# Performance work log

Hardware: AMD Instinct MI355X
Metric: run time of the kernel (lower is better)

Reference implementation:

```python
import jax, jax.numpy as jnp
import numpy as np

WS = 8
NH = 8
C = 192
HD = C // NH
SCALE = HD ** -0.5
EPS = 1e-5


def setup_inputs() -> dict:
    key = jax.random.key(0)
    ks = jax.random.split(key, 7)
    B, H, W = 8, 256, 256
    x = jax.random.normal(ks[0], (B, C, H, W), dtype=jnp.float32)
    gamma = jnp.ones((C,), dtype=jnp.float32)
    beta = jnp.zeros((C,), dtype=jnp.float32)
    w_qkv = jax.random.normal(ks[1], (C, 3 * C), dtype=jnp.float32) * (C ** -0.5)
    b_qkv = jnp.zeros((3 * C,), dtype=jnp.float32)
    w_proj = jax.random.normal(ks[2], (C, C), dtype=jnp.float32) * (C ** -0.5)
    b_proj = jnp.zeros((C,), dtype=jnp.float32)
    return {"x": x, "gamma": gamma, "beta": beta, "w_qkv": w_qkv,
            "b_qkv": b_qkv, "w_proj": w_proj, "b_proj": b_proj}


def reference(x, gamma, beta, w_qkv, b_qkv, w_proj, b_proj):
    B, Cc, H, W = x.shape
    # H, W chosen divisible by WS -> pad branch is a no-op
    nh, nw = H // WS, W // WS
    # window partition: [B,C,H,W] -> [B*nh*nw, WS*WS, C]
    xw = x.reshape(B, Cc, nh, WS, nw, WS)
    xw = xw.transpose(0, 2, 4, 3, 5, 1).reshape(-1, WS * WS, Cc)
    # LayerNorm over channel dim
    mu = xw.mean(axis=-1, keepdims=True)
    var = jnp.mean((xw - mu) ** 2, axis=-1, keepdims=True)
    xn = (xw - mu) * jax.lax.rsqrt(var + EPS) * gamma + beta
    # QKV projection -> [3, nWin, NH, S, HD]
    S = WS * WS
    qkv = (xn @ w_qkv + b_qkv).reshape(-1, S, 3, NH, HD)
    qkv = qkv.transpose(2, 0, 3, 1, 4)
    q, k, v = qkv[0], qkv[1], qkv[2]
    attn = jax.nn.softmax(jnp.einsum('whsd,whtd->whst', q, k) * SCALE, axis=-1)
    xa = jnp.einsum('whst,whtd->whsd', attn, v)
    xa = xa.transpose(0, 2, 1, 3).reshape(-1, S, Cc)
    xa = xa @ w_proj + b_proj
    # un-window: -> [B, C, H, W]
    xa = xa.reshape(B, nh, nw, WS, WS, Cc)
    xa = xa.transpose(0, 5, 1, 3, 2, 4).reshape(B, Cc, H, W)
    return jax.nn.sigmoid(xa.mean(axis=1, keepdims=True))
```

## Files before the change

kernel.cpp:

```cpp
#include <hip/hip_runtime.h>
#include <hip/hip_bf16.h>


typedef __attribute__((ext_vector_type(4))) float floatx4;
typedef __attribute__((ext_vector_type(8))) short short8;

#define SCALE_Q 0.20412414523193154f
#define LN_EPS 1e-5f

#define RXN 200
#define RQK 264
#define RPC 40
#define OFF_XN    0
#define OFF_Q     25600
#define OFF_K     59392
#define OFF_PC    93184
#define OFF_LOGIT 134144
#define OFF_VW    134400
#define LDS_BYTES 136448

__device__ __forceinline__ floatx4 mfma16(short8 a, short8 b, floatx4 c) {
  return __builtin_amdgcn_mfma_f32_16x16x32_bf16(a, b, c, 0, 0, 0);
}

__global__ void prep_kernel(const float* __restrict__ w_qkv,
                            const float* __restrict__ w_proj,
                            const float* __restrict__ b_proj,
                            __hip_bfloat16* __restrict__ wfrag,
                            float* __restrict__ wbar) {
  int tid = blockIdx.x * 256 + threadIdx.x;
  if (tid < 36 * 6 * 64) {
    int j = tid / 384, rem = tid % 384, ksr = rem / 64, l = rem % 64;
    int n  = 16 * j + (l & 15);
    int k0 = 32 * ksr + (l >> 4) * 8;
#pragma unroll
    for (int i = 0; i < 8; ++i)
      wfrag[(size_t)tid * 8 + i] = __float2bfloat16(w_qkv[(k0 + i) * 576 + n]);
  }
  if (tid < 192) {
    float s = 0.f;
    for (int c = 0; c < 192; ++c) s += w_proj[tid * 192 + c];
    wbar[tid] = s * (1.f / 192.f);
  } else if (tid == 192) {
    float s = 0.f;
    for (int c = 0; c < 192; ++c) s += b_proj[c];
    wbar[192] = s * (1.f / 192.f);
  }
}

__global__ __launch_bounds__(512, 2) void swin_kernel(
    const float* __restrict__ x,
    const float* __restrict__ gamma,
    const float* __restrict__ beta,
    const float* __restrict__ b_qkv,
    const __hip_bfloat16* __restrict__ wfrag,
    const float* __restrict__ wbar,
    float* __restrict__ out) {
  __shared__ __align__(16) char smem[LDS_BYTES];
  __hip_bfloat16* xn = (__hip_bfloat16*)(smem + OFF_XN);
  __hip_bfloat16* lq = (__hip_bfloat16*)(smem + OFF_Q);
  __hip_bfloat16* lk = (__hip_bfloat16*)(smem + OFF_K);
  float* logit = (float*)(smem + OFF_LOGIT);
  float* vwf   = (float*)(smem + OFF_VW);
  float2* scratch = (float2*)(smem + OFF_PC);

  const int tid = threadIdx.x;
  const int w   = tid >> 6;
  const int l   = tid & 63;
  const int l15 = l & 15;
  const int lg  = l >> 4;
  __hip_bfloat16* pcw = (__hip_bfloat16*)(smem + OFF_PC + w * (64 * RPC * 2));
  const floatx4 fzero = {0.f, 0.f, 0.f, 0.f};

  for (int i = tid; i < 64 * 64; i += 512) {
    int rr = i >> 6, hc = i & 63;
    int hh = hc >> 3, dd = 24 + (hc & 7);
    lq[rr * RQK + hh * 32 + dd] = __float2bfloat16(0.f);
    lk[rr * RQK + hh * 32 + dd] = __float2bfloat16(0.f);
  }
  if (tid < 64) logit[tid] = 0.f;
  vwf[tid] = 0.f;
  __syncthreads();

  const int p  = blockIdx.x;
  const int bb = p & 7;
  const int wh = p >> 3;
  const int tr = l >> 3, tc = l & 7;
  const int c0 = w * 24;
  const float* xb = x + (size_t)bb * 192 * 65536 + (size_t)(wh * 8 + tr) * 256 + tc;

  float xr[24];
#pragma unroll
  for (int i = 0; i < 24; ++i) xr[i] = xb[(size_t)(c0 + i) * 65536];

#pragma unroll 1
  for (int it = 0; it < 32; ++it) {
    float s1 = 0.f, s2 = 0.f;
#pragma unroll
    for (int i = 0; i < 24; ++i) { s1 += xr[i]; s2 += xr[i] * xr[i]; }
    scratch[w * 64 + l] = make_float2(s1, s2);
    __syncthreads();
    float ts = 0.f, tq = 0.f;
#pragma unroll
    for (int g = 0; g < 8; ++g) { float2 v = scratch[g * 64 + l]; ts += v.x; tq += v.y; }
    const float mu   = ts * (1.f / 192.f);
    const float rstd = rsqrtf(tq * (1.f / 192.f) - mu * mu + LN_EPS);
#pragma unroll
    for (int i = 0; i < 24; ++i) {
      float xv = (xr[i] - mu) * rstd * gamma[c0 + i] + beta[c0 + i];
      xn[l * RXN + c0 + i] = __float2bfloat16(xv);
    }
    __syncthreads();

    if (it < 31) {
#pragma unroll
      for (int i = 0; i < 24; ++i)
        xr[i] = xb[(size_t)(c0 + i) * 65536 + (it + 1) * 8];
    }

    short8 af[4][6];
#pragma unroll
    for (int mi = 0; mi < 4; ++mi)
#pragma unroll
      for (int ks = 0; ks < 6; ++ks)
        af[mi][ks] = *(const short8*)&xn[(16 * mi + l15) * RXN + 32 * ks + lg * 8];

    for (int j = w; j < 36; j += 8) {
      floatx4 aa[4];
#pragma unroll
      for (int mi = 0; mi < 4; ++mi) aa[mi] = fzero;
      const short8* bp = (const short8*)wfrag + (size_t)(j * 384 + l);
#pragma unroll
      for (int ks = 0; ks < 6; ++ks) {
        short8 bf = bp[ks * 64];
#pragma unroll
        for (int mi = 0; mi < 4; ++mi) aa[mi] = mfma16(af[mi][ks], bf, aa[mi]);
      }
      const int n = 16 * j + l15;
      const float bias = b_qkv[n];
      if (j < 12) {
        const int hh = n / 24, dd = n - hh * 24;
#pragma unroll
        for (int mi = 0; mi < 4; ++mi)
#pragma unroll
          for (int rg = 0; rg < 4; ++rg) {
            int t = 16 * mi + lg * 4 + rg;
            lq[t * RQK + hh * 32 + dd] = __float2bfloat16((aa[mi][rg] + bias) * SCALE_Q);
          }
      } else if (j < 24) {
        const int cc = n - 192;
        const int hh = cc / 24, dd = cc - hh * 24;
#pragma unroll
        for (int mi = 0; mi < 4; ++mi)
#pragma unroll
          for (int rg = 0; rg < 4; ++rg) {
            int t = 16 * mi + lg * 4 + rg;
            lk[t * RQK + hh * 32 + dd] = __float2bfloat16(aa[mi][rg] + bias);
          }
      } else {
        const int cc = n - 384;
        const int hh = cc / 24;
        const float wbv = wbar[cc];
        float part[16];
#pragma unroll
        for (int mi = 0; mi < 4; ++mi)
#pragma unroll
          for (int rg = 0; rg < 4; ++rg)
            part[mi * 4 + rg] = (aa[mi][rg] + bias) * wbv;
#pragma unroll
        for (int v2 = 0; v2 < 16; ++v2) {
          float t0 = part[v2];
          t0 += __shfl_xor(t0, 1);
          t0 += __shfl_xor(t0, 2);
          t0 += __shfl_xor(t0, 4);
          part[v2] = t0;
        }
        if ((l15 & 7) == 0) {
#pragma unroll
          for (int mi = 0; mi < 4; ++mi)
#pragma unroll
            for (int rg = 0; rg < 4; ++rg) {
              int t = 16 * mi + lg * 4 + rg;
              atomicAdd(&vwf[hh * 64 + t], part[mi * 4 + rg]);
            }
        }
      }
    }
    __syncthreads();

    {
      const int hh = w;
      short8 qf[4], kf[4];
#pragma unroll
      for (int i = 0; i < 4; ++i) {
        qf[i] = *(const short8*)&lq[(16 * i + l15) * RQK + hh * 32 + lg * 8];
        kf[i] = *(const short8*)&lk[(16 * i + l15) * RQK + hh * 32 + lg * 8];
      }
      floatx4 sc[4][4];
#pragma unroll
      for (int i = 0; i < 4; ++i)
#pragma unroll
        for (int j2 = 0; j2 < 4; ++j2)
          sc[i][j2] = mfma16(qf[i], kf[j2], fzero);
#pragma unroll
      for (int i = 0; i < 4; ++i)
#pragma unroll
        for (int j2 = 0; j2 < 4; ++j2)
#pragma unroll
          for (int rg = 0; rg < 4; ++rg)
            sc[i][j2][rg] = exp2f(sc[i][j2][rg] * 1.44269504f);

      short8 vwfrag[2], onesf;
#pragma unroll
      for (int q2 = 0; q2 < 8; ++q2) onesf[q2] = (short)0x3F80;
#pragma unroll
      for (int kc = 0; kc < 2; ++kc)
#pragma unroll
        for (int q2 = 0; q2 < 8; ++q2) {
          __hip_bfloat16 hb = __float2bfloat16(vwf[hh * 64 + kc * 32 + lg * 8 + q2]);
          short sv; __builtin_memcpy(&sv, &hb, 2);
          vwfrag[kc][q2] = sv;
        }

      floatx4 cacc[4], racc[4];
#pragma unroll
      for (int i = 0; i < 4; ++i) { cacc[i] = fzero; racc[i] = fzero; }
#pragma unroll
      for (int kc = 0; kc < 2; ++kc) {
#pragma unroll
        for (int i = 0; i < 4; ++i)
#pragma unroll
          for (int jj = 0; jj < 2; ++jj)
#pragma unroll
            for (int rg = 0; rg < 4; ++rg) {
              int row = 16 * i + lg * 4 + rg;
              pcw[row * RPC + jj * 16 + l15] = __float2bfloat16(sc[i][kc * 2 + jj][rg]);
            }
#pragma unroll
        for (int i = 0; i < 4; ++i) {
          short8 pf = *(const short8*)&pcw[(16 * i + l15) * RPC + lg * 8];
          cacc[i] = mfma16(pf, vwfrag[kc], cacc[i]);
          racc[i] = mfma16(pf, onesf, racc[i]);
        }
      }
      if (l15 == 0) {
#pragma unroll
        for (int i = 0; i < 4; ++i)
#pragma unroll
          for (int rg = 0; rg < 4; ++rg) {
            int row = 16 * i + lg * 4 + rg;
            atomicAdd(&logit[row], cacc[i][rg] / racc[i][rg]);
          }
      }
    }
    __syncthreads();

    if (tid < 64) {
      float vL = logit[tid] + wbar[192];
      out[(size_t)bb * 65536 + (size_t)(wh * 8 + (tid >> 3)) * 256 + it * 8 + (tid & 7)]
          = 1.f / (1.f + __expf(-vL));
      logit[tid] = 0.f;
    }
    vwf[tid] = 0.f;
  }
}

extern "C" void kernel_launch(void* const* d_in, const int* in_sizes, int n_in,
                              void* d_out, int out_size, void* d_ws, size_t ws_size,
                              hipStream_t stream) {
  const float* x      = (const float*)d_in[0];
  const float* gamma  = (const float*)d_in[1];
  const float* beta   = (const float*)d_in[2];
  const float* w_qkv  = (const float*)d_in[3];
  const float* b_qkv  = (const float*)d_in[4];
  const float* w_proj = (const float*)d_in[5];
  const float* b_proj = (const float*)d_in[6];
  float* out = (float*)d_out;

  __hip_bfloat16* wfrag = (__hip_bfloat16*)d_ws;
  float* wbar = (float*)((char*)d_ws + 221184);

  prep_kernel<<<54, 256, 0, stream>>>(w_qkv, w_proj, b_proj, wfrag, wbar);
  swin_kernel<<<256, 512, 0, stream>>>(x, gamma, beta, b_qkv, wfrag, wbar, out);
}
```

Before: 1.184 ms.

## Shrink LDS footprint, split row strips across more blocks, replace PV MFMA with shuffles

Aliases the normalized-input buffer onto the Q region and the LayerNorm scratch onto K, and drops the per-wave P staging buffer and logit buffer. This roughly halves LDS so more blocks fit per CU, and the launch-bounds hint is raised to match. The grid doubles by splitting each window row into two halves, giving 512 blocks instead of 256 on a large-CU GPU. The attention-times-vw reduction now uses FMAs and cross-lane shuffles instead of bf16 MFMA through LDS, the next-input prefetch moves after the QKV GEMM, and zero padding is rewritten every iteration. The risks are extra barriers per iteration and register pressure under the tighter occupancy bound.

```diff
diff --git a/kernel.cpp b/kernel.cpp
--- a/kernel.cpp
+++ b/kernel.cpp
@@ -10,14 +10,10 @@
 
 #define RXN 200
 #define RQK 264
-#define RPC 40
-#define OFF_XN    0
-#define OFF_Q     25600
-#define OFF_K     59392
-#define OFF_PC    93184
-#define OFF_LOGIT 134144
-#define OFF_VW    134400
-#define LDS_BYTES 136448
+#define OFF_Q  0
+#define OFF_K  33792
+#define OFF_VW 67584
+#define LDS_BYTES 69632
 
 __device__ __forceinline__ floatx4 mfma16(short8 a, short8 b, floatx4 c) {
   return __builtin_amdgcn_mfma_f32_16x16x32_bf16(a, b, c, 0, 0, 0);
@@ -48,7 +44,7 @@
   }
 }
 
-__global__ __launch_bounds__(512, 2) void swin_kernel(
+__global__ __launch_bounds__(512, 4) void swin_kernel(
     const float* __restrict__ x,
     const float* __restrict__ gamma,
     const float* __restrict__ beta,
@@ -57,44 +53,34 @@
     const float* __restrict__ wbar,
     float* __restrict__ out) {
   __shared__ __align__(16) char smem[LDS_BYTES];
-  __hip_bfloat16* xn = (__hip_bfloat16*)(smem + OFF_XN);
+  __hip_bfloat16* xn = (__hip_bfloat16*)(smem + OFF_Q);
   __hip_bfloat16* lq = (__hip_bfloat16*)(smem + OFF_Q);
   __hip_bfloat16* lk = (__hip_bfloat16*)(smem + OFF_K);
-  float* logit = (float*)(smem + OFF_LOGIT);
-  float* vwf   = (float*)(smem + OFF_VW);
-  float2* scratch = (float2*)(smem + OFF_PC);
+  float* vwf = (float*)(smem + OFF_VW);
+  float2* scratch = (float2*)(smem + OFF_K);
 
   const int tid = threadIdx.x;
   const int w   = tid >> 6;
   const int l   = tid & 63;
   const int l15 = l & 15;
   const int lg  = l >> 4;
-  __hip_bfloat16* pcw = (__hip_bfloat16*)(smem + OFF_PC + w * (64 * RPC * 2));
   const floatx4 fzero = {0.f, 0.f, 0.f, 0.f};
 
-  for (int i = tid; i < 64 * 64; i += 512) {
-    int rr = i >> 6, hc = i & 63;
-    int hh = hc >> 3, dd = 24 + (hc & 7);
-    lq[rr * RQK + hh * 32 + dd] = __float2bfloat16(0.f);
-    lk[rr * RQK + hh * 32 + dd] = __float2bfloat16(0.f);
-  }
-  if (tid < 64) logit[tid] = 0.f;
-  vwf[tid] = 0.f;
-  __syncthreads();
-
-  const int p  = blockIdx.x;
-  const int bb = p & 7;
-  const int wh = p >> 3;
+  const int p    = blockIdx.x;
+  const int bb   = p & 7;
+  const int wh   = (p >> 3) & 31;
+  const int hseg = p >> 8;
   const int tr = l >> 3, tc = l & 7;
   const int c0 = w * 24;
-  const float* xb = x + (size_t)bb * 192 * 65536 + (size_t)(wh * 8 + tr) * 256 + tc;
+  const float* xb = x + (size_t)bb * 192 * 65536 + (size_t)(wh * 8 + tr) * 256
+                      + hseg * 128 + tc;
 
   float xr[24];
 #pragma unroll
   for (int i = 0; i < 24; ++i) xr[i] = xb[(size_t)(c0 + i) * 65536];
 
 #pragma unroll 1
-  for (int it = 0; it < 32; ++it) {
+  for (int it = 0; it < 16; ++it) {
     float s1 = 0.f, s2 = 0.f;
 #pragma unroll
     for (int i = 0; i < 24; ++i) { s1 += xr[i]; s2 += xr[i] * xr[i]; }
@@ -103,6 +89,7 @@
     float ts = 0.f, tq = 0.f;
 #pragma unroll
     for (int g = 0; g < 8; ++g) { float2 v = scratch[g * 64 + l]; ts += v.x; tq += v.y; }
+    vwf[tid] = 0.f;
     const float mu   = ts * (1.f / 192.f);
     const float rstd = rsqrtf(tq * (1.f / 192.f) - mu * mu + LN_EPS);
 #pragma unroll
@@ -112,18 +99,23 @@
     }
     __syncthreads();
 
-    if (it < 31) {
-#pragma unroll
-      for (int i = 0; i < 24; ++i)
-        xr[i] = xb[(size_t)(c0 + i) * 65536 + (it + 1) * 8];
-    }
-
     short8 af[4][6];
 #pragma unroll
     for (int mi = 0; mi < 4; ++mi)
 #pragma unroll
       for (int ks = 0; ks < 6; ++ks)
         af[mi][ks] = *(const short8*)&xn[(16 * mi + l15) * RXN + 32 * ks + lg * 8];
+    __syncthreads();
+
+    {
+      const short8 zz = {0, 0, 0, 0, 0, 0, 0, 0};
+#pragma unroll
+      for (int i2 = tid; i2 < 1024; i2 += 512) {
+        int sel = i2 & 1, r2 = i2 >> 1;
+        __hip_bfloat16* dst = (sel ? lk : lq) + (r2 >> 3) * RQK + (r2 & 7) * 32 + 24;
+        *(short8*)dst = zz;
+      }
+    }
 
     for (int j = w; j < 36; j += 8) {
       floatx4 aa[4];
@@ -186,6 +178,12 @@
         }
       }
     }
+
+    if (it < 15) {
+#pragma unroll
+      for (int i = 0; i < 24; ++i)
+        xr[i] = xb[(size_t)(c0 + i) * 65536 + (it + 1) * 8];
+    }
     __syncthreads();
 
     {
@@ -196,6 +194,10 @@
         qf[i] = *(const short8*)&lq[(16 * i + l15) * RQK + hh * 32 + lg * 8];
         kf[i] = *(const short8*)&lk[(16 * i + l15) * RQK + hh * 32 + lg * 8];
       }
+      float vwv[4];
+#pragma unroll
+      for (int j2 = 0; j2 < 4; ++j2) vwv[j2] = vwf[hh * 64 + 16 * j2 + l15];
+
       floatx4 sc[4][4];
 #pragma unroll
       for (int i = 0; i < 4; ++i)
@@ -210,58 +212,40 @@
           for (int rg = 0; rg < 4; ++rg)
             sc[i][j2][rg] = exp2f(sc[i][j2][rg] * 1.44269504f);
 
-      short8 vwfrag[2], onesf;
-#pragma unroll
-      for (int q2 = 0; q2 < 8; ++q2) onesf[q2] = (short)0x3F80;
-#pragma unroll
-      for (int kc = 0; kc < 2; ++kc)
-#pragma unroll
-        for (int q2 = 0; q2 < 8; ++q2) {
-          __hip_bfloat16 hb = __float2bfloat16(vwf[hh * 64 + kc * 32 + lg * 8 + q2]);
-          short sv; __builtin_memcpy(&sv, &hb, 2);
-          vwfrag[kc][q2] = sv;
-        }
-
-      floatx4 cacc[4], racc[4];
-#pragma unroll
-      for (int i = 0; i < 4; ++i) { cacc[i] = fzero; racc[i] = fzero; }
-#pragma unroll
-      for (int kc = 0; kc < 2; ++kc) {
-#pragma unroll
-        for (int i = 0; i < 4; ++i)
-#pragma unroll
-          for (int jj = 0; jj < 2; ++jj)
-#pragma unroll
-            for (int rg = 0; rg < 4; ++rg) {
-              int row = 16 * i + lg * 4 + rg;
-              pcw[row * RPC + jj * 16 + l15] = __float2bfloat16(sc[i][kc * 2 + jj][rg]);
-            }
-#pragma unroll
-        for (int i = 0; i < 4; ++i) {
-          short8 pf = *(const short8*)&pcw[(16 * i + l15) * RPC + lg * 8];
-          cacc[i] = mfma16(pf, vwfrag[kc], cacc[i]);
-          racc[i] = mfma16(pf, onesf, racc[i]);
-        }
-      }
-      if (l15 == 0) {
-#pragma unroll
-        for (int i = 0; i < 4; ++i)
-#pragma unroll
-          for (int rg = 0; rg < 4; ++rg) {
-            int row = 16 * i + lg * 4 + rg;
-            atomicAdd(&logit[row], cacc[i][rg] / racc[i][rg]);
-          }
+#pragma unroll
+      for (int i = 0; i < 4; ++i) {
+        float num[4] = {0.f, 0.f, 0.f, 0.f};
+        float den[4] = {0.f, 0.f, 0.f, 0.f};
+#pragma unroll
+        for (int j2 = 0; j2 < 4; ++j2)
+#pragma unroll
+          for (int rg = 0; rg < 4; ++rg) {
+            float pv = sc[i][j2][rg];
+            den[rg] += pv;
+            num[rg] = fmaf(pv, vwv[j2], num[rg]);
+          }
+#pragma unroll
+        for (int m = 1; m < 16; m <<= 1)
+#pragma unroll
+          for (int rg = 0; rg < 4; ++rg) {
+            num[rg] += __shfl_xor(num[rg], m);
+            den[rg] += __shfl_xor(den[rg], m);
+          }
+#pragma unroll
+        for (int rg = 0; rg < 4; ++rg)
+          if (l15 == i * 4 + rg)
+            vwf[hh * 64 + 16 * i + lg * 4 + rg] = __fdividef(num[rg], den[rg]);
       }
     }
     __syncthreads();
 
     if (tid < 64) {
-      float vL = logit[tid] + wbar[192];
-      out[(size_t)bb * 65536 + (size_t)(wh * 8 + (tid >> 3)) * 256 + it * 8 + (tid & 7)]
-          = 1.f / (1.f + __expf(-vL));
-      logit[tid] = 0.f;
-    }
-    vwf[tid] = 0.f;
+      float vL = wbar[192];
+#pragma unroll
+      for (int h8 = 0; h8 < 8; ++h8) vL += vwf[h8 * 64 + tid];
+      out[(size_t)bb * 65536 + (size_t)(wh * 8 + (tid >> 3)) * 256
+          + hseg * 128 + it * 8 + (tid & 7)] = 1.f / (1.f + __expf(-vL));
+    }
   }
 }
 
@@ -281,5 +265,5 @@
   float* wbar = (float*)((char*)d_ws + 221184);
 
   prep_kernel<<<54, 256, 0, stream>>>(w_qkv, w_proj, b_proj, wfrag, wbar);
-  swin_kernel<<<256, 512, 0, stream>>>(x, gamma, beta, b_qkv, wfrag, wbar, out);
-}
+  swin_kernel<<<512, 512, 0, stream>>>(x, gamma, beta, b_qkv, wfrag, wbar, out);
+}
```

Result: slower. 1.647 ms (+39.1%).
